# Optimization experiments

Hardware: AMD Instinct MI355X
Metric: run time of the kernel (lower is better)

## Reference

```python
import jax, jax.numpy as jnp
import numpy as np

NHEAD = 8
DMODEL = 512
DK = DMODEL // NHEAD  # 64

def setup_inputs() -> dict:
    key = jax.random.key(0)
    ks = jax.random.split(key, 7)
    B, S = 4, 2048
    Q = jax.random.normal(ks[0], (B, S, DMODEL), dtype=jnp.float32)
    K = jax.random.normal(ks[1], (B, S, DMODEL), dtype=jnp.float32)
    V = jax.random.normal(ks[2], (B, S, DMODEL), dtype=jnp.float32)
    # Original uses torch.rand (uniform [0,1)) for all weights.
    WQ = jax.random.uniform(ks[3], (NHEAD, DMODEL, DK), dtype=jnp.float32)
    WK = jax.random.uniform(ks[4], (NHEAD, DMODEL, DK), dtype=jnp.float32)
    WV = jax.random.uniform(ks[5], (NHEAD, DMODEL, DK), dtype=jnp.float32)
    WO = jax.random.uniform(ks[6], (NHEAD * DK, DMODEL), dtype=jnp.float32)
    return {"Q": Q, "K": K, "V": V, "WQ": WQ, "WK": WK, "WV": WV, "WO": WO}

def reference(Q, K, V, WQ, WK, WV, WO):
    # Stacked per-head projections: [B,H,S,dk]
    Qh = jnp.einsum('bsd,hdk->bhsk', Q, WQ)
    Kh = jnp.einsum('bsd,hdk->bhsk', K, WK)
    Vh = jnp.einsum('bsd,hdk->bhsk', V, WV)
    dk = Kh.shape[-1]
    scores = jnp.einsum('bhqk,bhsk->bhqs', Qh, Kh) / jnp.sqrt(jnp.float32(dk))
    attn = jax.nn.softmax(scores, axis=-1)  # dropout omitted (eval / deterministic baseline)
    out = jnp.einsum('bhqs,bhsk->bhqk', attn, Vh)
    B, H, S, Dk = out.shape
    out = out.transpose(0, 2, 1, 3).reshape(B, S, H * Dk)  # concat heads on last dim
    return out @ WO
```

## Files before the change

kernel.cpp:

```cpp
#include <hip/hip_runtime.h>

#define NB 4
#define NS 2048
#define ND 512
#define NH 8
#define NDK 64

typedef __attribute__((ext_vector_type(8))) short bf16x8;
typedef __attribute__((ext_vector_type(4))) float f32x4;

__device__ inline f32x4 mfma16(bf16x8 a, bf16x8 b, f32x4 c) {
    return __builtin_amdgcn_mfma_f32_16x16x32_bf16(a, b, c, 0, 0, 0);
}

__device__ inline unsigned short f2bf(float f) {
    unsigned u = __float_as_uint(f);
    unsigned r = u + 0x7FFFu + ((u >> 16) & 1u);
    return (unsigned short)(r >> 16);
}
__device__ inline float bf2f(unsigned short h) {
    return __uint_as_float(((unsigned)h) << 16);
}
__device__ inline void splitf(float x, short& hi, short& lo) {
    unsigned short h = f2bf(x);
    hi = (short)h;
    lo = (short)f2bf(x - bf2f(h));
}

__global__ __launch_bounds__(256) void proj_kernel(
    const float* __restrict__ Q, const float* __restrict__ K, const float* __restrict__ V,
    const float* __restrict__ WQ, const float* __restrict__ WK, const float* __restrict__ WV,
    short* __restrict__ qhi, short* __restrict__ qlo,
    short* __restrict__ khi, short* __restrict__ klo,
    short* __restrict__ vt)
{
    const int mt = blockIdx.x;
    const int h  = blockIdx.y;
    const int z  = blockIdx.z;
    const int m0 = mt * 128;
    const int tid = threadIdx.x;
    const int w = tid >> 6, lane = tid & 63, c = lane & 15, g = lane >> 4;

    const float* X = (z == 0) ? Q : (z == 1) ? K : V;
    const float* W = ((z == 0) ? WQ : (z == 1) ? WK : WV) + (size_t)h * ND * NDK;

    __shared__ __align__(16) short smem[15360];
    short* xhi  = smem;
    short* xlo  = smem + 5120;
    short* wthi = smem + 10240;
    short* wtlo = smem + 12800;

    f32x4 acc[2][4];
    #pragma unroll
    for (int i = 0; i < 2; i++)
        #pragma unroll
        for (int j = 0; j < 4; j++) acc[i][j] = f32x4{0.f, 0.f, 0.f, 0.f};

    for (int k0 = 0; k0 < ND; k0 += 32) {
        {
            int r = tid >> 1, kq = (tid & 1) * 16;
            const float* src = X + (size_t)(m0 + r) * ND + k0 + kq;
            short hv[16], lv[16];
            #pragma unroll
            for (int i = 0; i < 4; i++) {
                float4 f = ((const float4*)src)[i];
                splitf(f.x, hv[4*i+0], lv[4*i+0]);
                splitf(f.y, hv[4*i+1], lv[4*i+1]);
                splitf(f.z, hv[4*i+2], lv[4*i+2]);
                splitf(f.w, hv[4*i+3], lv[4*i+3]);
            }
            bf16x8 vh0, vh1, vl0, vl1;
            #pragma unroll
            for (int i = 0; i < 8; i++) { vh0[i]=hv[i]; vh1[i]=hv[8+i]; vl0[i]=lv[i]; vl1[i]=lv[8+i]; }
            *(bf16x8*)&xhi[r*40 + kq]     = vh0;
            *(bf16x8*)&xhi[r*40 + kq + 8] = vh1;
            *(bf16x8*)&xlo[r*40 + kq]     = vl0;
            *(bf16x8*)&xlo[r*40 + kq + 8] = vl1;
        }
        #pragma unroll
        for (int i = 0; i < 2; i++) {
            int idx = tid * 2 + i;
            int kr = idx >> 4, c4 = (idx & 15) * 4;
            float4 f = *(const float4*)(W + (size_t)(k0 + kr) * NDK + c4);
            short hh, ll;
            splitf(f.x, hh, ll); wthi[(c4+0)*40 + kr] = hh; wtlo[(c4+0)*40 + kr] = ll;
            splitf(f.y, hh, ll); wthi[(c4+1)*40 + kr] = hh; wtlo[(c4+1)*40 + kr] = ll;
            splitf(f.z, hh, ll); wthi[(c4+2)*40 + kr] = hh; wtlo[(c4+2)*40 + kr] = ll;
            splitf(f.w, hh, ll); wthi[(c4+3)*40 + kr] = hh; wtlo[(c4+3)*40 + kr] = ll;
        }
        __syncthreads();

        bf16x8 ah[2], al[2];
        ah[0] = *(bf16x8*)&xhi[(32*w +      c)*40 + 8*g];
        ah[1] = *(bf16x8*)&xhi[(32*w + 16 + c)*40 + 8*g];
        al[0] = *(bf16x8*)&xlo[(32*w +      c)*40 + 8*g];
        al[1] = *(bf16x8*)&xlo[(32*w + 16 + c)*40 + 8*g];
        #pragma unroll
        for (int nf = 0; nf < 4; nf++) {
            bf16x8 bh = *(bf16x8*)&wthi[(c + 16*nf)*40 + 8*g];
            bf16x8 bl = *(bf16x8*)&wtlo[(c + 16*nf)*40 + 8*g];
            #pragma unroll
            for (int mi = 0; mi < 2; mi++) {
                acc[mi][nf] = mfma16(ah[mi], bh, acc[mi][nf]);
                if (z < 2) {
                    acc[mi][nf] = mfma16(ah[mi], bl, acc[mi][nf]);
                    acc[mi][nf] = mfma16(al[mi], bh, acc[mi][nf]);
                }
            }
        }
        __syncthreads();
    }

    if (z < 2) {
        short* ohi = (z == 0) ? qhi : khi;
        short* olo = (z == 0) ? qlo : klo;
        #pragma unroll
        for (int mi = 0; mi < 2; mi++)
            #pragma unroll
            for (int nf = 0; nf < 4; nf++)
                #pragma unroll
                for (int r = 0; r < 4; r++) {
                    int row = m0 + 32*w + 16*mi + 4*g + r;
                    int b = row >> 11, s = row & 2047;
                    int col = c + 16*nf;
                    size_t o = ((size_t)(b * NH + h) * NS + s) * NDK + col;
                    short hh, ll; splitf(acc[mi][nf][r], hh, ll);
                    ohi[o] = hh; olo[o] = ll;
                }
    } else {
        short* vtile = smem;
        #pragma unroll
        for (int mi = 0; mi < 2; mi++)
            #pragma unroll
            for (int nf = 0; nf < 4; nf++)
                #pragma unroll
                for (int r = 0; r < 4; r++) {
                    int rl = 32*w + 16*mi + 4*g + r;
                    vtile[rl*72 + c + 16*nf] = (short)f2bf(acc[mi][nf][r]);
                }
        __syncthreads();
        int dk = tid >> 2, sc4 = (tid & 3) * 32;
        int b = m0 >> 11;
        int sbase = (m0 & 2047) + sc4;
        short* dst = vt + ((size_t)(b * NH + h) * NDK + dk) * NS + sbase;
        #pragma unroll
        for (int ch = 0; ch < 4; ch++) {
            bf16x8 vv;
            #pragma unroll
            for (int i = 0; i < 8; i++) vv[i] = vtile[(sc4 + ch*8 + i)*72 + dk];
            *(bf16x8*)&dst[ch*8] = vv;
        }
    }
}

__global__ __launch_bounds__(256) void attn_kernel(
    const short* __restrict__ qhi, const short* __restrict__ qlo,
    const short* __restrict__ khi, const short* __restrict__ klo,
    const short* __restrict__ vt, short* __restrict__ ao)
{
    const int bh = blockIdx.x;
    const int qb = blockIdx.y * 64;
    const int tid = threadIdx.x;
    const int w = tid >> 6, lane = tid & 63, c = lane & 15, g = lane >> 4;

    __shared__ __align__(16) short kldsh[64*72];
    __shared__ __align__(16) short kldsl[64*72];
    __shared__ __align__(16) short vlds [64*72];
    __shared__ __align__(16) short pbuf [4*16*72];
    short* pw = pbuf + w * 16 * 72;

    bf16x8 qh[2], ql[2];
    {
        const size_t qrow = ((size_t)bh * NS + qb + 16*w + c) * NDK;
        qh[0] = *(const bf16x8*)&qhi[qrow + 8*g];
        qh[1] = *(const bf16x8*)&qhi[qrow + 32 + 8*g];
        ql[0] = *(const bf16x8*)&qlo[qrow + 8*g];
        ql[1] = *(const bf16x8*)&qlo[qrow + 32 + 8*g];
    }

    float mrow[4], lrow[4];
    f32x4 acc[4];
    #pragma unroll
    for (int r = 0; r < 4; r++) { mrow[r] = -1e30f; lrow[r] = 0.f; }
    #pragma unroll
    for (int nf = 0; nf < 4; nf++) acc[nf] = f32x4{0.f, 0.f, 0.f, 0.f};

    for (int s0 = 0; s0 < NS; s0 += 64) {
        {
            int row = tid >> 2, cq = (tid & 3) * 16;
            size_t go = ((size_t)bh * NS + s0 + row) * NDK + cq;
            *(bf16x8*)&kldsh[row*72 + cq]     = *(const bf16x8*)&khi[go];
            *(bf16x8*)&kldsh[row*72 + cq + 8] = *(const bf16x8*)&khi[go + 8];
            *(bf16x8*)&kldsl[row*72 + cq]     = *(const bf16x8*)&klo[go];
            *(bf16x8*)&kldsl[row*72 + cq + 8] = *(const bf16x8*)&klo[go + 8];
            size_t gv = ((size_t)bh * NDK + row) * NS + s0 + cq;
            *(bf16x8*)&vlds[row*72 + cq]      = *(const bf16x8*)&vt[gv];
            *(bf16x8*)&vlds[row*72 + cq + 8]  = *(const bf16x8*)&vt[gv + 8];
        }
        __syncthreads();

        f32x4 sc[4];
        #pragma unroll
        for (int sf = 0; sf < 4; sf++) {
            sc[sf] = f32x4{0.f, 0.f, 0.f, 0.f};
            #pragma unroll
            for (int ks = 0; ks < 2; ks++) {
                bf16x8 kh = *(bf16x8*)&kldsh[(c + 16*sf)*72 + ks*32 + 8*g];
                bf16x8 kl = *(bf16x8*)&kldsl[(c + 16*sf)*72 + ks*32 + 8*g];
                sc[sf] = mfma16(qh[ks], kh, sc[sf]);
                sc[sf] = mfma16(qh[ks], kl, sc[sf]);
                sc[sf] = mfma16(ql[ks], kh, sc[sf]);
            }
        }

        float mnew[4], fac[4], rs[4];
        #pragma unroll
        for (int r = 0; r < 4; r++) {
            float v = -1e30f;
            #pragma unroll
            for (int sf = 0; sf < 4; sf++) { sc[sf][r] *= 0.125f; v = fmaxf(v, sc[sf][r]); }
            #pragma unroll
            for (int off = 1; off < 16; off <<= 1) v = fmaxf(v, __shfl_xor(v, off));
            mnew[r] = fmaxf(mrow[r], v);
            fac[r]  = __expf(mrow[r] - mnew[r]);
            mrow[r] = mnew[r];
            rs[r] = 0.f;
        }
        #pragma unroll
        for (int sf = 0; sf < 4; sf++)
            #pragma unroll
            for (int r = 0; r < 4; r++) {
                float p = __expf(sc[sf][r] - mnew[r]);
                rs[r] += p;
                pw[(4*g + r)*72 + c + 16*sf] = (short)f2bf(p);
            }
        #pragma unroll
        for (int r = 0; r < 4; r++) {
            float t = rs[r];
            #pragma unroll
            for (int off = 1; off < 16; off <<= 1) t += __shfl_xor(t, off);
            lrow[r] = lrow[r] * fac[r] + t;
        }
        #pragma unroll
        for (int nf = 0; nf < 4; nf++)
            #pragma unroll
            for (int r = 0; r < 4; r++) acc[nf][r] *= fac[r];

        #pragma unroll
        for (int ks = 0; ks < 2; ks++) {
            bf16x8 pa = *(bf16x8*)&pw[c*72 + ks*32 + 8*g];
            #pragma unroll
            for (int nf = 0; nf < 4; nf++) {
                bf16x8 vv = *(bf16x8*)&vlds[(c + 16*nf)*72 + ks*32 + 8*g];
                acc[nf] = mfma16(pa, vv, acc[nf]);
            }
        }
        __syncthreads();
    }

    const int b = bh >> 3, h = bh & 7;
    #pragma unroll
    for (int r = 0; r < 4; r++) {
        float inv = 1.f / lrow[r];
        int q = qb + 16*w + 4*g + r;
        size_t o = ((size_t)b * NS + q) * ND + h * NDK;
        #pragma unroll
        for (int nf = 0; nf < 4; nf++)
            ao[o + c + 16*nf] = (short)f2bf(acc[nf][r] * inv);
    }
}

__global__ __launch_bounds__(256) void oproj_kernel(
    const short* __restrict__ ao, const float* __restrict__ WO, float* __restrict__ out)
{
    const int mb = blockIdx.x * 128, nb = blockIdx.y * 64;
    const int tid = threadIdx.x;
    const int w = tid >> 6, lane = tid & 63, c = lane & 15, g = lane >> 4;

    __shared__ __align__(16) short xlds[128*40];
    __shared__ __align__(16) short wt[64*40];

    f32x4 acc[2][4];
    #pragma unroll
    for (int i = 0; i < 2; i++)
        #pragma unroll
        for (int j = 0; j < 4; j++) acc[i][j] = f32x4{0.f, 0.f, 0.f, 0.f};

    for (int k0 = 0; k0 < ND; k0 += 32) {
        {
            int r = tid >> 1, kq = (tid & 1) * 16;
            const short* src = ao + (size_t)(mb + r) * ND + k0 + kq;
            *(bf16x8*)&xlds[r*40 + kq]     = *(const bf16x8*)src;
            *(bf16x8*)&xlds[r*40 + kq + 8] = *(const bf16x8*)(src + 8);
        }
        #pragma unroll
        for (int i = 0; i < 2; i++) {
            int idx = tid * 2 + i;
            int kr = idx >> 4, c4 = (idx & 15) * 4;
            float4 f = *(const float4*)&WO[(size_t)(k0 + kr) * ND + nb + c4];
            wt[(c4+0)*40 + kr] = (short)f2bf(f.x);
            wt[(c4+1)*40 + kr] = (short)f2bf(f.y);
            wt[(c4+2)*40 + kr] = (short)f2bf(f.z);
            wt[(c4+3)*40 + kr] = (short)f2bf(f.w);
        }
        __syncthreads();
        bf16x8 a0 = *(bf16x8*)&xlds[(32*w +      c)*40 + 8*g];
        bf16x8 a1 = *(bf16x8*)&xlds[(32*w + 16 + c)*40 + 8*g];
        #pragma unroll
        for (int nf = 0; nf < 4; nf++) {
            bf16x8 bv = *(bf16x8*)&wt[(c + 16*nf)*40 + 8*g];
            acc[0][nf] = mfma16(a0, bv, acc[0][nf]);
            acc[1][nf] = mfma16(a1, bv, acc[1][nf]);
        }
        __syncthreads();
    }
    #pragma unroll
    for (int mi = 0; mi < 2; mi++)
        #pragma unroll
        for (int nf = 0; nf < 4; nf++)
            #pragma unroll
            for (int r = 0; r < 4; r++) {
                int row = mb + 32*w + 16*mi + 4*g + r;
                out[(size_t)row * ND + nb + c + 16*nf] = acc[mi][nf][r];
            }
}

extern "C" void kernel_launch(void* const* d_in, const int* in_sizes, int n_in,
                              void* d_out, int out_size, void* d_ws, size_t ws_size,
                              hipStream_t stream) {
    (void)in_sizes; (void)n_in; (void)out_size; (void)ws_size;
    const float* Q  = (const float*)d_in[0];
    const float* K  = (const float*)d_in[1];
    const float* V  = (const float*)d_in[2];
    const float* WQ = (const float*)d_in[3];
    const float* WK = (const float*)d_in[4];
    const float* WV = (const float*)d_in[5];
    const float* WO = (const float*)d_in[6];

    char* ws = (char*)d_ws;
    const size_t PLANE = (size_t)NB * NH * NS * NDK * 2;
    short* qhi = (short*)(ws);
    short* qlo = (short*)(ws + PLANE);
    short* khi = (short*)(ws + 2*PLANE);
    short* klo = (short*)(ws + 3*PLANE);
    short* vt  = (short*)(ws + 4*PLANE);
    short* ao  = (short*)(ws + 5*PLANE);

    proj_kernel<<<dim3(64, NH, 3), 256, 0, stream>>>(Q, K, V, WQ, WK, WV,
                                                     qhi, qlo, khi, klo, vt);
    attn_kernel<<<dim3(NB*NH, NS/64), 256, 0, stream>>>(qhi, qlo, khi, klo, vt, ao);
    oproj_kernel<<<dim3(64, ND/NDK), 256, 0, stream>>>(ao, WO, (float*)d_out);
}
```

Measured before the change: 327.9 us.

## Pre-split inputs, swizzled tiled K/V layout, async LDS loads, lazy softmax rescale

Adds a prep kernel that splits Q and K into bf16 hi/lo planes once, so the projection kernel no longer re-splits each input row for every head. Projections are now launched per tensor, with block-index remapping for cache locality. K and V are written as 64-row tiles with an XOR-swizzled layout, which lets the attention kernel load them straight into LDS with global_load_lds and without padding or bank conflicts. The softmax now works in the exp2 domain using v_exp_f32, truncates P to bf16 instead of rounding, and skips the running-max rescale unless the new max exceeds the old one by more than 12. The change adds kernel launches and extra memory traffic for the split planes, and the loose rescale threshold risks a small loss of accuracy.

```diff
diff --git a/kernel.cpp b/kernel.cpp
--- a/kernel.cpp
+++ b/kernel.cpp
@@ -7,12 +7,12 @@
 #define NDK 64
 
 typedef __attribute__((ext_vector_type(8))) short bf16x8;
+typedef __attribute__((ext_vector_type(4))) short bf16x4;
 typedef __attribute__((ext_vector_type(4))) float f32x4;
 
 __device__ inline f32x4 mfma16(bf16x8 a, bf16x8 b, f32x4 c) {
     return __builtin_amdgcn_mfma_f32_16x16x32_bf16(a, b, c, 0, 0, 0);
 }
-
 __device__ inline unsigned short f2bf(float f) {
     unsigned u = __float_as_uint(f);
     unsigned r = u + 0x7FFFu + ((u >> 16) & 1u);
@@ -26,94 +26,122 @@
     hi = (short)h;
     lo = (short)f2bf(x - bf2f(h));
 }
+__device__ inline float exp2_fast(float x) {
+    float r; asm("v_exp_f32 %0, %1" : "=v"(r) : "v"(x)); return r;
+}
+__device__ inline void gload16(const void* g, void* l) {
+    __builtin_amdgcn_global_load_lds(
+        (const __attribute__((address_space(1))) unsigned int*)g,
+        (__attribute__((address_space(3))) unsigned int*)l, 16, 0, 0);
+}
+
+__global__ __launch_bounds__(256) void prep_split(
+    const float* __restrict__ X, short* __restrict__ xh, short* __restrict__ xl)
+{
+    int i = (blockIdx.x * 256 + threadIdx.x) * 4;
+    float4 f = *(const float4*)(X + i);
+    short h0,h1,h2,h3,l0,l1,l2,l3;
+    splitf(f.x,h0,l0); splitf(f.y,h1,l1); splitf(f.z,h2,l2); splitf(f.w,h3,l3);
+    bf16x4 hv = {h0,h1,h2,h3}, lv = {l0,l1,l2,l3};
+    *(bf16x4*)(xh + i) = hv;
+    *(bf16x4*)(xl + i) = lv;
+}
 
 __global__ __launch_bounds__(256) void proj_kernel(
-    const float* __restrict__ Q, const float* __restrict__ K, const float* __restrict__ V,
-    const float* __restrict__ WQ, const float* __restrict__ WK, const float* __restrict__ WV,
-    short* __restrict__ qhi, short* __restrict__ qlo,
-    short* __restrict__ khi, short* __restrict__ klo,
-    short* __restrict__ vt)
+    const short* __restrict__ xh, const short* __restrict__ xl,
+    const float* __restrict__ xf, const float* __restrict__ Wf,
+    short* __restrict__ o1, short* __restrict__ o2, int z)
 {
-    const int mt = blockIdx.x;
-    const int h  = blockIdx.y;
-    const int z  = blockIdx.z;
+    const int orig = blockIdx.x;
+    const int wg = (orig & 7) * 64 + (orig >> 3);
+    const int mt = wg >> 3, h = wg & 7;
     const int m0 = mt * 128;
     const int tid = threadIdx.x;
     const int w = tid >> 6, lane = tid & 63, c = lane & 15, g = lane >> 4;
-
-    const float* X = (z == 0) ? Q : (z == 1) ? K : V;
-    const float* W = ((z == 0) ? WQ : (z == 1) ? WK : WV) + (size_t)h * ND * NDK;
+    const float* Wp = Wf + (size_t)h * ND * NDK;
 
     __shared__ __align__(16) short smem[15360];
-    short* xhi  = smem;
-    short* xlo  = smem + 5120;
-    short* wthi = smem + 10240;
-    short* wtlo = smem + 12800;
+    short* sxh = smem;
+    short* sxl = smem + 5120;
+    short* swh = smem + 10240;
+    short* swl = smem + 12800;
 
     f32x4 acc[2][4];
     #pragma unroll
     for (int i = 0; i < 2; i++)
         #pragma unroll
-        for (int j = 0; j < 4; j++) acc[i][j] = f32x4{0.f, 0.f, 0.f, 0.f};
+        for (int j = 0; j < 4; j++) acc[i][j] = f32x4{0.f,0.f,0.f,0.f};
 
     for (int k0 = 0; k0 < ND; k0 += 32) {
         {
             int r = tid >> 1, kq = (tid & 1) * 16;
-            const float* src = X + (size_t)(m0 + r) * ND + k0 + kq;
-            short hv[16], lv[16];
-            #pragma unroll
-            for (int i = 0; i < 4; i++) {
-                float4 f = ((const float4*)src)[i];
-                splitf(f.x, hv[4*i+0], lv[4*i+0]);
-                splitf(f.y, hv[4*i+1], lv[4*i+1]);
-                splitf(f.z, hv[4*i+2], lv[4*i+2]);
-                splitf(f.w, hv[4*i+3], lv[4*i+3]);
-            }
-            bf16x8 vh0, vh1, vl0, vl1;
-            #pragma unroll
-            for (int i = 0; i < 8; i++) { vh0[i]=hv[i]; vh1[i]=hv[8+i]; vl0[i]=lv[i]; vl1[i]=lv[8+i]; }
-            *(bf16x8*)&xhi[r*40 + kq]     = vh0;
-            *(bf16x8*)&xhi[r*40 + kq + 8] = vh1;
-            *(bf16x8*)&xlo[r*40 + kq]     = vl0;
-            *(bf16x8*)&xlo[r*40 + kq + 8] = vl1;
+            if (z < 2) {
+                const short* s1 = xh + (size_t)(m0 + r) * ND + k0 + kq;
+                const short* s2 = xl + (size_t)(m0 + r) * ND + k0 + kq;
+                *(bf16x8*)&sxh[r*40 + kq]     = *(const bf16x8*)s1;
+                *(bf16x8*)&sxh[r*40 + kq + 8] = *(const bf16x8*)(s1 + 8);
+                *(bf16x8*)&sxl[r*40 + kq]     = *(const bf16x8*)s2;
+                *(bf16x8*)&sxl[r*40 + kq + 8] = *(const bf16x8*)(s2 + 8);
+            } else {
+                const float* s1 = xf + (size_t)(m0 + r) * ND + k0 + kq;
+                short tmp[16];
+                #pragma unroll
+                for (int j = 0; j < 4; j++) {
+                    float4 f = ((const float4*)s1)[j];
+                    tmp[4*j+0] = (short)f2bf(f.x); tmp[4*j+1] = (short)f2bf(f.y);
+                    tmp[4*j+2] = (short)f2bf(f.z); tmp[4*j+3] = (short)f2bf(f.w);
+                }
+                bf16x8 v0, v1;
+                #pragma unroll
+                for (int j = 0; j < 8; j++) { v0[j] = tmp[j]; v1[j] = tmp[8+j]; }
+                *(bf16x8*)&sxh[r*40 + kq]     = v0;
+                *(bf16x8*)&sxh[r*40 + kq + 8] = v1;
+            }
         }
         #pragma unroll
         for (int i = 0; i < 2; i++) {
             int idx = tid * 2 + i;
             int kr = idx >> 4, c4 = (idx & 15) * 4;
-            float4 f = *(const float4*)(W + (size_t)(k0 + kr) * NDK + c4);
-            short hh, ll;
-            splitf(f.x, hh, ll); wthi[(c4+0)*40 + kr] = hh; wtlo[(c4+0)*40 + kr] = ll;
-            splitf(f.y, hh, ll); wthi[(c4+1)*40 + kr] = hh; wtlo[(c4+1)*40 + kr] = ll;
-            splitf(f.z, hh, ll); wthi[(c4+2)*40 + kr] = hh; wtlo[(c4+2)*40 + kr] = ll;
-            splitf(f.w, hh, ll); wthi[(c4+3)*40 + kr] = hh; wtlo[(c4+3)*40 + kr] = ll;
-        }
-        __syncthreads();
-
-        bf16x8 ah[2], al[2];
-        ah[0] = *(bf16x8*)&xhi[(32*w +      c)*40 + 8*g];
-        ah[1] = *(bf16x8*)&xhi[(32*w + 16 + c)*40 + 8*g];
-        al[0] = *(bf16x8*)&xlo[(32*w +      c)*40 + 8*g];
-        al[1] = *(bf16x8*)&xlo[(32*w + 16 + c)*40 + 8*g];
+            float4 f = *(const float4*)(Wp + (size_t)(k0 + kr) * NDK + c4);
+            if (z < 2) {
+                short hh, ll;
+                splitf(f.x, hh, ll); swh[(c4+0)*40 + kr] = hh; swl[(c4+0)*40 + kr] = ll;
+                splitf(f.y, hh, ll); swh[(c4+1)*40 + kr] = hh; swl[(c4+1)*40 + kr] = ll;
+                splitf(f.z, hh, ll); swh[(c4+2)*40 + kr] = hh; swl[(c4+2)*40 + kr] = ll;
+                splitf(f.w, hh, ll); swh[(c4+3)*40 + kr] = hh; swl[(c4+3)*40 + kr] = ll;
+            } else {
+                swh[(c4+0)*40 + kr] = (short)f2bf(f.x);
+                swh[(c4+1)*40 + kr] = (short)f2bf(f.y);
+                swh[(c4+2)*40 + kr] = (short)f2bf(f.z);
+                swh[(c4+3)*40 + kr] = (short)f2bf(f.w);
+            }
+        }
+        __syncthreads();
+
+        bf16x8 ah0 = *(bf16x8*)&sxh[(32*w +      c)*40 + 8*g];
+        bf16x8 ah1 = *(bf16x8*)&sxh[(32*w + 16 + c)*40 + 8*g];
+        bf16x8 al0, al1;
+        if (z < 2) {
+            al0 = *(bf16x8*)&sxl[(32*w +      c)*40 + 8*g];
+            al1 = *(bf16x8*)&sxl[(32*w + 16 + c)*40 + 8*g];
+        }
         #pragma unroll
         for (int nf = 0; nf < 4; nf++) {
-            bf16x8 bh = *(bf16x8*)&wthi[(c + 16*nf)*40 + 8*g];
-            bf16x8 bl = *(bf16x8*)&wtlo[(c + 16*nf)*40 + 8*g];
-            #pragma unroll
-            for (int mi = 0; mi < 2; mi++) {
-                acc[mi][nf] = mfma16(ah[mi], bh, acc[mi][nf]);
-                if (z < 2) {
-                    acc[mi][nf] = mfma16(ah[mi], bl, acc[mi][nf]);
-                    acc[mi][nf] = mfma16(al[mi], bh, acc[mi][nf]);
-                }
-            }
-        }
-        __syncthreads();
-    }
-
-    if (z < 2) {
-        short* ohi = (z == 0) ? qhi : khi;
-        short* olo = (z == 0) ? qlo : klo;
+            bf16x8 bh = *(bf16x8*)&swh[(c + 16*nf)*40 + 8*g];
+            acc[0][nf] = mfma16(ah0, bh, acc[0][nf]);
+            acc[1][nf] = mfma16(ah1, bh, acc[1][nf]);
+            if (z < 2) {
+                bf16x8 bl = *(bf16x8*)&swl[(c + 16*nf)*40 + 8*g];
+                acc[0][nf] = mfma16(ah0, bl, acc[0][nf]);
+                acc[1][nf] = mfma16(ah1, bl, acc[1][nf]);
+                acc[0][nf] = mfma16(al0, bh, acc[0][nf]);
+                acc[1][nf] = mfma16(al1, bh, acc[1][nf]);
+            }
+        }
+        __syncthreads();
+    }
+
+    if (z == 0) {
         #pragma unroll
         for (int mi = 0; mi < 2; mi++)
             #pragma unroll
@@ -121,14 +149,43 @@
                 #pragma unroll
                 for (int r = 0; r < 4; r++) {
                     int row = m0 + 32*w + 16*mi + 4*g + r;
-                    int b = row >> 11, s = row & 2047;
-                    int col = c + 16*nf;
-                    size_t o = ((size_t)(b * NH + h) * NS + s) * NDK + col;
+                    int b_ = row >> 11, s = row & 2047;
+                    size_t o = ((size_t)(b_ * NH + h) * NS + s) * NDK + c + 16*nf;
                     short hh, ll; splitf(acc[mi][nf][r], hh, ll);
-                    ohi[o] = hh; olo[o] = ll;
+                    o1[o] = hh; o2[o] = ll;
                 }
+    } else if (z == 1) {
+        const int bh = (m0 >> 11) * NH + h;
+        short* ep = smem;
+        #pragma unroll
+        for (int pass = 0; pass < 2; pass++) {
+            __syncthreads();
+            #pragma unroll
+            for (int mi = 0; mi < 2; mi++)
+                #pragma unroll
+                for (int nf = 0; nf < 4; nf++)
+                    #pragma unroll
+                    for (int r = 0; r < 4; r++) {
+                        int rl = 32*w + 16*mi + 4*g + r;
+                        short hh, ll; splitf(acc[mi][nf][r], hh, ll);
+                        ep[rl*72 + c + 16*nf] = pass ? ll : hh;
+                    }
+            __syncthreads();
+            int rl = tid >> 1, half = tid & 1;
+            int s = (m0 & 2047) + rl;
+            int t = s >> 6, sr = s & 63;
+            char* op = (char*)(pass ? o2 : o1) + ((size_t)bh * 32 + t) * 8192 + sr * 128;
+            int sw = (sr & 7) << 4;
+            #pragma unroll
+            for (int ch = 0; ch < 4; ch++) {
+                bf16x8 vv = *(bf16x8*)&ep[rl*72 + half*32 + ch*8];
+                *(bf16x8*)(op + ((half*64 + ch*16) ^ sw)) = vv;
+            }
+        }
     } else {
-        short* vtile = smem;
+        const int bh = (m0 >> 11) * NH + h;
+        short* ep = smem;
+        __syncthreads();
         #pragma unroll
         for (int mi = 0; mi < 2; mi++)
             #pragma unroll
@@ -136,38 +193,43 @@
                 #pragma unroll
                 for (int r = 0; r < 4; r++) {
                     int rl = 32*w + 16*mi + 4*g + r;
-                    vtile[rl*72 + c + 16*nf] = (short)f2bf(acc[mi][nf][r]);
+                    ep[rl*72 + c + 16*nf] = (short)f2bf(acc[mi][nf][r]);
                 }
         __syncthreads();
-        int dk = tid >> 2, sc4 = (tid & 3) * 32;
-        int b = m0 >> 11;
-        int sbase = (m0 & 2047) + sc4;
-        short* dst = vt + ((size_t)(b * NH + h) * NDK + dk) * NS + sbase;
+        int dk = tid >> 2, scq = (tid & 3) * 32;
         #pragma unroll
         for (int ch = 0; ch < 4; ch++) {
+            int sl = scq + ch*8;
+            int s = (m0 & 2047) + sl;
+            int t = s >> 6, sr0 = s & 63;
             bf16x8 vv;
             #pragma unroll
-            for (int i = 0; i < 8; i++) vv[i] = vtile[(sc4 + ch*8 + i)*72 + dk];
-            *(bf16x8*)&dst[ch*8] = vv;
+            for (int i = 0; i < 8; i++) vv[i] = ep[(sl + i)*72 + dk];
+            char* op = (char*)o1 + ((size_t)bh * 32 + t) * 8192 + dk * 128;
+            *(bf16x8*)(op + ((2*sr0) ^ ((dk & 7) << 4))) = vv;
         }
     }
 }
 
 __global__ __launch_bounds__(256) void attn_kernel(
     const short* __restrict__ qhi, const short* __restrict__ qlo,
-    const short* __restrict__ khi, const short* __restrict__ klo,
-    const short* __restrict__ vt, short* __restrict__ ao)
+    const short* __restrict__ kth, const short* __restrict__ ktl,
+    const short* __restrict__ vtl, short* __restrict__ ao)
 {
-    const int bh = blockIdx.x;
-    const int qb = blockIdx.y * 64;
+    const int orig = blockIdx.x;
+    const int wg = (orig & 7) * 128 + (orig >> 3);
+    const int bh = wg >> 5, qb = (wg & 31) * 64;
     const int tid = threadIdx.x;
     const int w = tid >> 6, lane = tid & 63, c = lane & 15, g = lane >> 4;
 
-    __shared__ __align__(16) short kldsh[64*72];
-    __shared__ __align__(16) short kldsl[64*72];
-    __shared__ __align__(16) short vlds [64*72];
-    __shared__ __align__(16) short pbuf [4*16*72];
-    short* pw = pbuf + w * 16 * 72;
+    __shared__ __align__(16) short kh_s[64*64];
+    __shared__ __align__(16) short kl_s[64*64];
+    __shared__ __align__(16) short v_s [64*64];
+    __shared__ __align__(16) short pb  [4][16*64];
+    char* khb = (char*)kh_s;
+    char* klb = (char*)kl_s;
+    char* vb  = (char*)v_s;
+    char* pwb = (char*)pb[w];
 
     bf16x8 qh[2], ql[2];
     {
@@ -178,92 +240,105 @@
         ql[1] = *(const bf16x8*)&qlo[qrow + 32 + 8*g];
     }
 
+    const char* ktb = (const char*)kth + (size_t)bh * 32 * 8192;
+    const char* klg = (const char*)ktl + (size_t)bh * 32 * 8192;
+    const char* vtb = (const char*)vtl + (size_t)bh * 32 * 8192;
+
+    const float SC = 0.18033688f;
     float mrow[4], lrow[4];
     f32x4 acc[4];
     #pragma unroll
     for (int r = 0; r < 4; r++) { mrow[r] = -1e30f; lrow[r] = 0.f; }
     #pragma unroll
-    for (int nf = 0; nf < 4; nf++) acc[nf] = f32x4{0.f, 0.f, 0.f, 0.f};
-
-    for (int s0 = 0; s0 < NS; s0 += 64) {
-        {
-            int row = tid >> 2, cq = (tid & 3) * 16;
-            size_t go = ((size_t)bh * NS + s0 + row) * NDK + cq;
-            *(bf16x8*)&kldsh[row*72 + cq]     = *(const bf16x8*)&khi[go];
-            *(bf16x8*)&kldsh[row*72 + cq + 8] = *(const bf16x8*)&khi[go + 8];
-            *(bf16x8*)&kldsl[row*72 + cq]     = *(const bf16x8*)&klo[go];
-            *(bf16x8*)&kldsl[row*72 + cq + 8] = *(const bf16x8*)&klo[go + 8];
-            size_t gv = ((size_t)bh * NDK + row) * NS + s0 + cq;
-            *(bf16x8*)&vlds[row*72 + cq]      = *(const bf16x8*)&vt[gv];
-            *(bf16x8*)&vlds[row*72 + cq + 8]  = *(const bf16x8*)&vt[gv + 8];
-        }
+    for (int nf = 0; nf < 4; nf++) acc[nf] = f32x4{0.f,0.f,0.f,0.f};
+
+    for (int t = 0; t < 32; ++t) {
+        size_t toff = (size_t)t * 8192 + w * 2048 + lane * 16;
+        gload16(ktb + toff,        (char*)kh_s + w*2048);
+        gload16(ktb + toff + 1024, (char*)kh_s + w*2048 + 1024);
+        gload16(klg + toff,        (char*)kl_s + w*2048);
+        gload16(klg + toff + 1024, (char*)kl_s + w*2048 + 1024);
+        gload16(vtb + toff,        (char*)v_s  + w*2048);
+        gload16(vtb + toff + 1024, (char*)v_s  + w*2048 + 1024);
         __syncthreads();
 
         f32x4 sc[4];
         #pragma unroll
         for (int sf = 0; sf < 4; sf++) {
-            sc[sf] = f32x4{0.f, 0.f, 0.f, 0.f};
+            sc[sf] = f32x4{0.f,0.f,0.f,0.f};
+            int rowK = c + 16*sf;
             #pragma unroll
             for (int ks = 0; ks < 2; ks++) {
-                bf16x8 kh = *(bf16x8*)&kldsh[(c + 16*sf)*72 + ks*32 + 8*g];
-                bf16x8 kl = *(bf16x8*)&kldsl[(c + 16*sf)*72 + ks*32 + 8*g];
+                int cb = (ks*64 + 16*g) ^ ((rowK & 7) << 4);
+                bf16x8 kh = *(bf16x8*)(khb + rowK*128 + cb);
+                bf16x8 kl = *(bf16x8*)(klb + rowK*128 + cb);
                 sc[sf] = mfma16(qh[ks], kh, sc[sf]);
                 sc[sf] = mfma16(qh[ks], kl, sc[sf]);
                 sc[sf] = mfma16(ql[ks], kh, sc[sf]);
             }
         }
 
-        float mnew[4], fac[4], rs[4];
+        float tmax[4];
         #pragma unroll
         for (int r = 0; r < 4; r++) {
-            float v = -1e30f;
-            #pragma unroll
-            for (int sf = 0; sf < 4; sf++) { sc[sf][r] *= 0.125f; v = fmaxf(v, sc[sf][r]); }
+            sc[0][r] *= SC; sc[1][r] *= SC; sc[2][r] *= SC; sc[3][r] *= SC;
+            float v = fmaxf(fmaxf(sc[0][r], sc[1][r]), fmaxf(sc[2][r], sc[3][r]));
             #pragma unroll
             for (int off = 1; off < 16; off <<= 1) v = fmaxf(v, __shfl_xor(v, off));
-            mnew[r] = fmaxf(mrow[r], v);
-            fac[r]  = __expf(mrow[r] - mnew[r]);
-            mrow[r] = mnew[r];
-            rs[r] = 0.f;
-        }
-        #pragma unroll
-        for (int sf = 0; sf < 4; sf++)
+            tmax[r] = v;
+        }
+        bool need = (tmax[0] > mrow[0] + 12.f) || (tmax[1] > mrow[1] + 12.f) ||
+                    (tmax[2] > mrow[2] + 12.f) || (tmax[3] > mrow[3] + 12.f);
+        if (__any(need)) {
             #pragma unroll
             for (int r = 0; r < 4; r++) {
-                float p = __expf(sc[sf][r] - mnew[r]);
+                float mn = fmaxf(mrow[r], tmax[r]);
+                float fc = exp2_fast(mrow[r] - mn);
+                mrow[r] = mn; lrow[r] *= fc;
+                acc[0][r] *= fc; acc[1][r] *= fc; acc[2][r] *= fc; acc[3][r] *= fc;
+            }
+        }
+        float rs[4] = {0.f,0.f,0.f,0.f};
+        #pragma unroll
+        for (int sf = 0; sf < 4; sf++) {
+            #pragma unroll
+            for (int r = 0; r < 4; r++) {
+                float p = exp2_fast(sc[sf][r] - mrow[r]);
                 rs[r] += p;
-                pw[(4*g + r)*72 + c + 16*sf] = (short)f2bf(p);
-            }
+                int q = 4*g + r;
+                *(short*)(pwb + q*128 + ((2*c + 32*sf) ^ ((q & 7) << 4))) =
+                    (short)(__float_as_uint(p) >> 16);
+            }
+        }
         #pragma unroll
         for (int r = 0; r < 4; r++) {
-            float t = rs[r];
-            #pragma unroll
-            for (int off = 1; off < 16; off <<= 1) t += __shfl_xor(t, off);
-            lrow[r] = lrow[r] * fac[r] + t;
-        }
-        #pragma unroll
-        for (int nf = 0; nf < 4; nf++)
-            #pragma unroll
-            for (int r = 0; r < 4; r++) acc[nf][r] *= fac[r];
+            float t2 = rs[r];
+            #pragma unroll
+            for (int off = 1; off < 16; off <<= 1) t2 += __shfl_xor(t2, off);
+            lrow[r] += t2;
+        }
 
         #pragma unroll
         for (int ks = 0; ks < 2; ks++) {
-            bf16x8 pa = *(bf16x8*)&pw[c*72 + ks*32 + 8*g];
+            int cbp = (ks*64 + 16*g) ^ ((c & 7) << 4);
+            bf16x8 pa = *(bf16x8*)(pwb + c*128 + cbp);
             #pragma unroll
             for (int nf = 0; nf < 4; nf++) {
-                bf16x8 vv = *(bf16x8*)&vlds[(c + 16*nf)*72 + ks*32 + 8*g];
+                int rowV = c + 16*nf;
+                int cbv = (ks*64 + 16*g) ^ ((rowV & 7) << 4);
+                bf16x8 vv = *(bf16x8*)(vb + rowV*128 + cbv);
                 acc[nf] = mfma16(pa, vv, acc[nf]);
             }
         }
         __syncthreads();
     }
 
-    const int b = bh >> 3, h = bh & 7;
+    const int b = bh >> 3, hh = bh & 7;
     #pragma unroll
     for (int r = 0; r < 4; r++) {
         float inv = 1.f / lrow[r];
         int q = qb + 16*w + 4*g + r;
-        size_t o = ((size_t)b * NS + q) * ND + h * NDK;
+        size_t o = ((size_t)b * NS + q) * ND + hh * NDK;
         #pragma unroll
         for (int nf = 0; nf < 4; nf++)
             ao[o + c + 16*nf] = (short)f2bf(acc[nf][r] * inv);
@@ -273,7 +348,9 @@
 __global__ __launch_bounds__(256) void oproj_kernel(
     const short* __restrict__ ao, const float* __restrict__ WO, float* __restrict__ out)
 {
-    const int mb = blockIdx.x * 128, nb = blockIdx.y * 64;
+    const int orig = blockIdx.x;
+    const int wg = (orig & 7) * 64 + (orig >> 3);
+    const int mb = (wg >> 3) * 128, nb = (wg & 7) * 64;
     const int tid = threadIdx.x;
     const int w = tid >> 6, lane = tid & 63, c = lane & 15, g = lane >> 4;
 
@@ -284,7 +361,7 @@
     #pragma unroll
     for (int i = 0; i < 2; i++)
         #pragma unroll
-        for (int j = 0; j < 4; j++) acc[i][j] = f32x4{0.f, 0.f, 0.f, 0.f};
+        for (int j = 0; j < 4; j++) acc[i][j] = f32x4{0.f,0.f,0.f,0.f};
 
     for (int k0 = 0; k0 < ND; k0 += 32) {
         {
@@ -339,15 +416,20 @@
 
     char* ws = (char*)d_ws;
     const size_t PLANE = (size_t)NB * NH * NS * NDK * 2;
-    short* qhi = (short*)(ws);
-    short* qlo = (short*)(ws + PLANE);
-    short* khi = (short*)(ws + 2*PLANE);
-    short* klo = (short*)(ws + 3*PLANE);
-    short* vt  = (short*)(ws + 4*PLANE);
-    short* ao  = (short*)(ws + 5*PLANE);
-
-    proj_kernel<<<dim3(64, NH, 3), 256, 0, stream>>>(Q, K, V, WQ, WK, WV,
-                                                     qhi, qlo, khi, klo, vt);
-    attn_kernel<<<dim3(NB*NH, NS/64), 256, 0, stream>>>(qhi, qlo, khi, klo, vt, ao);
-    oproj_kernel<<<dim3(64, ND/NDK), 256, 0, stream>>>(ao, WO, (float*)d_out);
-}
+    short* xh    = (short*)(ws);
+    short* xl    = (short*)(ws +   PLANE);
+    short* qhi   = (short*)(ws + 2*PLANE);
+    short* qlo   = (short*)(ws + 3*PLANE);
+    short* kth   = (short*)(ws + 4*PLANE);
+    short* ktl   = (short*)(ws + 5*PLANE);
+    short* vtile = xh;
+    short* ao    = xl;
+
+    prep_split<<<4096, 256, 0, stream>>>(Q, xh, xl);
+    proj_kernel<<<512, 256, 0, stream>>>(xh, xl, nullptr, WQ, qhi, qlo, 0);
+    prep_split<<<4096, 256, 0, stream>>>(K, xh, xl);
+    proj_kernel<<<512, 256, 0, stream>>>(xh, xl, nullptr, WK, kth, ktl, 1);
+    proj_kernel<<<512, 256, 0, stream>>>(nullptr, nullptr, V, WV, vtile, nullptr, 2);
+    attn_kernel<<<1024, 256, 0, stream>>>(qhi, qlo, kth, ktl, vtile, ao);
+    oproj_kernel<<<512, 256, 0, stream>>>(ao, WO, (float*)d_out);
+}
```

Result: slower. 361.5 us (+10.2%).
